# Performance work log

Measured on AMD Instinct MI355X. Metric: run time of the kernel, lower is better.

Reference implementation:

```python
import jax, jax.numpy as jnp
import numpy as np

N_NODES = 50000
N_EDGES = 800000
N_GRAPHS = 512
IN_DIM = 128
HID = 64
NLAYERS = 3
BN_EPS = 1e-5
NEG_SLOPE = 0.2


def setup_inputs() -> dict:
    key = jax.random.key(0)
    ks = jax.random.split(key, 16)
    s = 0.1  # weight scale
    x = jax.random.normal(ks[0], (N_NODES, IN_DIM), jnp.float32)
    ei_sc = jax.random.randint(ks[1], (2, N_EDGES), 0, N_NODES, dtype=jnp.int32)
    ei_fc = jax.random.randint(ks[2], (2, N_EDGES), 0, N_NODES, dtype=jnp.int32)
    batch_ids = jnp.sort(jax.random.randint(ks[3], (N_NODES,), 0, N_GRAPHS, dtype=jnp.int32))
    return {
        "x": x,
        "ei_sc": ei_sc,
        "ei_fc": ei_fc,
        "batch_ids": batch_ids,
        "Ws": jax.random.normal(ks[4], (NLAYERS, IN_DIM, 2 * HID), jnp.float32) * s,
        "att_src": jax.random.normal(ks[5], (NLAYERS, 2, HID), jnp.float32) * s,
        "att_dst": jax.random.normal(ks[6], (NLAYERS, 2, HID), jnp.float32) * s,
        "bgat": jnp.zeros((NLAYERS, 2 * HID), jnp.float32),
        "bn_g": jnp.ones((NLAYERS, 2 * HID), jnp.float32),
        "bn_b": jnp.zeros((NLAYERS, 2 * HID), jnp.float32),
        "Wf": jax.random.normal(ks[7], (2 * HID, HID), jnp.float32) * s,
        "af_src": jax.random.normal(ks[8], (1, HID), jnp.float32) * s,
        "af_dst": jax.random.normal(ks[9], (1, HID), jnp.float32) * s,
        "bf": jnp.zeros((HID,), jnp.float32),
        "Wo": jax.random.normal(ks[10], (HID, 1), jnp.float32) * s,
        "bo": jnp.zeros((1,), jnp.float32),
    }


def gat_conv(x, src, dst, W, a_src, a_dst, b):
    """PyG GATConv: linear -> per-head attention logits -> dst-segment softmax -> scatter-sum."""
    N = x.shape[0]
    H, C = a_src.shape
    h = (x @ W).reshape(N, H, C)                      # [N,H,C]
    loop = jnp.arange(N, dtype=src.dtype)             # add self-loops (PyG default)
    s = jnp.concatenate([src, loop])
    d = jnp.concatenate([dst, loop])
    al_s = jnp.einsum('nhc,hc->nh', h, a_src)         # [N,H]
    al_d = jnp.einsum('nhc,hc->nh', h, a_dst)
    al = jax.nn.leaky_relu(al_s[s] + al_d[d], NEG_SLOPE)  # [E,H]
    m = jax.ops.segment_max(al, d, num_segments=N)
    m = jnp.where(jnp.isfinite(m), m, 0.0)
    e = jnp.exp(al - m[d])
    denom = jax.ops.segment_sum(e, d, num_segments=N)
    coef = e / (denom[d] + 1e-16)                     # softmax over incoming edges
    out = jax.ops.segment_sum(coef[:, :, None] * h[s], d, num_segments=N)  # [N,H,C]
    return out.reshape(N, H * C) + b                  # concat heads + bias


def batch_norm(x, g, b):
    mu = x.mean(axis=0)
    var = ((x - mu) ** 2).mean(axis=0)                # biased var, as torch BN train-mode
    return (x - mu) * jax.lax.rsqrt(var + BN_EPS) * g + b


def reference(x, ei_sc, ei_fc, batch_ids, Ws, att_src, att_dst, bgat,
              bn_g, bn_b, Wf, af_src, af_dst, bf, Wo, bo):
    x0 = x
    x1 = x
    for l in range(NLAYERS):
        x0 = gat_conv(x0, ei_sc[0], ei_sc[1], Ws[l], att_src[l], att_dst[l], bgat[l])
        x1 = gat_conv(x1, ei_fc[0], ei_fc[1], Ws[l], att_src[l], att_dst[l], bgat[l])
        x0 = jax.nn.relu(batch_norm(x0, bn_g[l], bn_b[l]))
        x1 = jax.nn.relu(batch_norm(x1, bn_g[l], bn_b[l]))
        # Dropout: identity (eval mode, deterministic reference)
    x0 = gat_conv(x0, ei_sc[0], ei_sc[1], Wf, af_src, af_dst, bf)
    x1 = gat_conv(x1, ei_fc[0], ei_fc[1], Wf, af_src, af_dst, bf)
    xf = (x0 + x1) * 0.5                              # reduce_fuse_embed='mean'
    out = xf @ Wo + bo                                # [N, nclass]
    sums = jax.ops.segment_sum(out, batch_ids, num_segments=N_GRAPHS)
    cnts = jax.ops.segment_sum(jnp.ones((out.shape[0], 1), out.dtype), batch_ids, num_segments=N_GRAPHS)
    return sums / jnp.maximum(cnts, 1.0)              # scatter mean over graphs -> [G, nclass]
```

## Files before the change

kernel.cpp:

```cpp
#include <hip/hip_runtime.h>
#include <cstdint>
#include <cstddef>


#define NLAYERS 3
#define BN_BLOCKS 256

__device__ __forceinline__ float lrelu(float a){ return a > 0.f ? a : 0.2f*a; }

__device__ __forceinline__ float wsum(float v){
#pragma unroll
  for (int o = 32; o > 0; o >>= 1) v += __shfl_xor(v, o);
  return v;
}

__global__ void zero_k(int* __restrict__ p, int n){
  int i = blockIdx.x*blockDim.x + threadIdx.x;
  if (i < n) p[i] = 0;
}
__global__ void copy_k(const int* __restrict__ a, int* __restrict__ b, int n){
  int i = blockIdx.x*blockDim.x + threadIdx.x;
  if (i < n) b[i] = a[i];
}
__global__ void count_k(const int* __restrict__ dst, int E, int* __restrict__ cnt){
  int e = blockIdx.x*blockDim.x + threadIdx.x;
  if (e < E) atomicAdd(&cnt[dst[e]], 1);
}
__global__ __launch_bounds__(1024) void scanA_k(const int* __restrict__ cnt,
    int* __restrict__ excl, int* __restrict__ bsum, int N){
  __shared__ int wpart[16];
  const int tid = threadIdx.x, lane = tid & 63, w = tid >> 6;
  const int i = blockIdx.x*1024 + tid;
  const int v = (i < N) ? cnt[i] : 0;
  int s = v;
#pragma unroll
  for (int o = 1; o < 64; o <<= 1){ int t = __shfl_up(s, o); if (lane >= o) s += t; }
  if (lane == 63) wpart[w] = s;
  __syncthreads();
  if (w == 0){
    int t = (lane < 16) ? wpart[lane] : 0;
#pragma unroll
    for (int o = 1; o < 16; o <<= 1){ int u = __shfl_up(t, o); if (lane >= o) t += u; }
    if (lane < 16) wpart[lane] = t;
  }
  __syncthreads();
  const int woff = (w > 0) ? wpart[w-1] : 0;
  const int incl = s + woff;
  if (i < N) excl[i] = incl - v;
  if (tid == 1023) bsum[blockIdx.x] = incl;
}
__global__ void scanB_k(const int* __restrict__ bsum, int* __restrict__ boff, int nb){
  const int lane = threadIdx.x;
  const int v = (lane < nb) ? bsum[lane] : 0;
  int s = v;
#pragma unroll
  for (int o = 1; o < 64; o <<= 1){ int t = __shfl_up(s, o); if (lane >= o) s += t; }
  if (lane < nb) boff[lane] = s - v;
  if (lane == nb-1) boff[nb] = s;
}
__global__ __launch_bounds__(1024) void scanC_k(int* __restrict__ rp,
    const int* __restrict__ boff, int N, int nb){
  const int i = blockIdx.x*1024 + threadIdx.x;
  if (i < N) rp[i] += boff[blockIdx.x];
  if (i == 0) rp[N] = boff[nb];
}
__global__ void fill_k(const int* __restrict__ src, const int* __restrict__ dst, int E,
                       int* __restrict__ pos, int* __restrict__ col){
  int e = blockIdx.x*blockDim.x + threadIdx.x;
  if (e < E){
    int d = dst[e];
    int p = atomicAdd(&pos[d], 1);
    col[p] = src[e];
  }
}
__global__ __launch_bounds__(256) void sortrow_k(const int* __restrict__ rp,
                                                 int* __restrict__ col, int N){
  const int lane = threadIdx.x & 63;
  const int n = blockIdx.x*4 + (threadIdx.x >> 6);
  if (n >= N) return;
  const int b = rp[n], e = rp[n+1];
  const int deg = e - b;
  if (deg <= 1) return;
  if (deg <= 64){
    int v = (lane < deg) ? col[b + lane] : 0x7fffffff;
#pragma unroll
    for (int k = 2; k <= 64; k <<= 1){
#pragma unroll
      for (int j = k >> 1; j > 0; j >>= 1){
        const int other = __shfl_xor(v, j);
        const bool up = ((lane & k) == 0);
        const bool takeMin = (((lane & j) == 0) == up);
        v = takeMin ? min(v, other) : max(v, other);
      }
    }
    if (lane < deg) col[b + lane] = v;
  } else if (lane == 0){
    for (int i = b + 1; i < e; ++i){
      const int key = col[i];
      int j = i - 1;
      while (j >= b && col[j] > key){ col[j+1] = col[j]; --j; }
      col[j+1] = key;
    }
  }
}

__global__ __launch_bounds__(256) void gemm_k(const float* __restrict__ A,
    const float* __restrict__ W, float* __restrict__ O,
    const float* __restrict__ bnsc, const float* __restrict__ bnsh,
    const float* __restrict__ atts, const float* __restrict__ attd,
    float* __restrict__ als, float* __restrict__ ald, int N, int M){
  __shared__ float xs[64][64];
  __shared__ float wsh[64][64];
  const int tid = threadIdx.x;
  const int row0 = blockIdx.x*64, col0 = blockIdx.y*64;
  const int HS = gridDim.y;
  const int ty = tid >> 4, tx = tid & 15;
  float acc[4][4] = {};

  for (int kk = 0; kk < 128; kk += 64){
    {
      const int c4 = (tid & 15)*4;
#pragma unroll
      for (int p = 0; p < 4; ++p){
        const int k = p*16 + (tid >> 4);
        *reinterpret_cast<float4*>(&wsh[k][c4]) =
            *reinterpret_cast<const float4*>(&W[(size_t)(kk + k)*M + col0 + c4]);
      }
    }
    {
      const int k4 = (tid & 15)*4;
      const int rbase = tid >> 4;
#pragma unroll
      for (int p = 0; p < 4; ++p){
        const int rr = p*16 + rbase;
        int gr = row0 + rr; if (gr > N-1) gr = N-1;
        float4 xv = *reinterpret_cast<const float4*>(&A[(size_t)gr*128 + kk + k4]);
        float xq[4] = {xv.x, xv.y, xv.z, xv.w};
        if (bnsc != nullptr){
#pragma unroll
          for (int q = 0; q < 4; ++q)
            xq[q] = fmaxf(xq[q]*bnsc[kk + k4 + q] + bnsh[kk + k4 + q], 0.f);
        }
#pragma unroll
        for (int q = 0; q < 4; ++q){
          const int k = k4 + q;
          const int swz = ((k >> 2) & 15) << 2;
          xs[k][rr ^ swz] = xq[q];
        }
      }
    }
    __syncthreads();
#pragma unroll 8
    for (int k = 0; k < 64; ++k){
      const int swz = ((k >> 2) & 15) << 2;
      const int xr = (ty*4) ^ swz;
      const float4 xv = *reinterpret_cast<const float4*>(&xs[k][xr]);
      const float2 w0 = *reinterpret_cast<const float2*>(&wsh[k][2*tx]);
      const float2 w1 = *reinterpret_cast<const float2*>(&wsh[k][32 + 2*tx]);
      const float xq[4] = {xv.x, xv.y, xv.z, xv.w};
#pragma unroll
      for (int i = 0; i < 4; ++i){
        acc[i][0] += xq[i]*w0.x;
        acc[i][1] += xq[i]*w0.y;
        acc[i][2] += xq[i]*w1.x;
        acc[i][3] += xq[i]*w1.y;
      }
    }
    __syncthreads();
  }
  {
    const float* as = atts + col0;
    const float* ad = attd + col0;
    const float a_s0 = as[2*tx],      a_s1 = as[2*tx + 1];
    const float a_s2 = as[32 + 2*tx], a_s3 = as[33 + 2*tx];
    const float a_d0 = ad[2*tx],      a_d1 = ad[2*tx + 1];
    const float a_d2 = ad[32 + 2*tx], a_d3 = ad[33 + 2*tx];
#pragma unroll
    for (int i = 0; i < 4; ++i){
      float ps = acc[i][0]*a_s0 + acc[i][1]*a_s1 + acc[i][2]*a_s2 + acc[i][3]*a_s3;
      float pd = acc[i][0]*a_d0 + acc[i][1]*a_d1 + acc[i][2]*a_d2 + acc[i][3]*a_d3;
#pragma unroll
      for (int o = 1; o < 16; o <<= 1){
        ps += __shfl_xor(ps, o);
        pd += __shfl_xor(pd, o);
      }
      const int r = row0 + ty*4 + i;
      if (tx == 0 && r < N){
        als[(size_t)r*HS + blockIdx.y] = ps;
        ald[(size_t)r*HS + blockIdx.y] = pd;
      }
    }
  }
#pragma unroll
  for (int i = 0; i < 4; ++i){
    const int r = row0 + ty*4 + i;
    if (r < N){
      float2* o2 = reinterpret_cast<float2*>(&O[(size_t)r*M + col0]);
      o2[tx]      = make_float2(acc[i][0], acc[i][1]);
      o2[16 + tx] = make_float2(acc[i][2], acc[i][3]);
    }
  }
}

template<int H>
__global__ __launch_bounds__(256) void agg_k(const float* __restrict__ h,
    const float* __restrict__ als, const float* __restrict__ ald,
    const int* __restrict__ rp, const int* __restrict__ col,
    const float* __restrict__ bias, float* __restrict__ out, int N){
  const int lane = threadIdx.x & 63;
  const int n = blockIdx.x*4 + (threadIdx.x >> 6);
  if (n >= N) return;
  const int beg = rp[n], end = rp[n+1];
  float as0, as1 = 0.f, ad0, ad1 = 0.f;
  if (H == 2){
    const float2 a = ((const float2*)als)[n];
    const float2 d = ((const float2*)ald)[n];
    as0 = a.x; as1 = a.y; ad0 = d.x; ad1 = d.y;
  } else { as0 = als[n]; ad0 = ald[n]; }
  const float self0 = lrelu(as0 + ad0);
  const float self1 = (H == 2) ? lrelu(as1 + ad1) : 0.f;
  float m0 = self0, p0 = (lane == 0) ? 1.f : 0.f;
  float m1 = self1, p1 = (lane == 0) ? 1.f : 0.f;
  for (int i = beg + lane; i < end; i += 64){
    const int s = col[i];
    if (H == 2){
      const float2 a = ((const float2*)als)[s];
      const float al0 = lrelu(a.x + ad0);
      const float al1 = lrelu(a.y + ad1);
      if (al0 > m0){ p0 = p0*__expf(m0 - al0) + 1.f; m0 = al0; }
      else p0 += __expf(al0 - m0);
      if (al1 > m1){ p1 = p1*__expf(m1 - al1) + 1.f; m1 = al1; }
      else p1 += __expf(al1 - m1);
    } else {
      const float al0 = lrelu(als[s] + ad0);
      if (al0 > m0){ p0 = p0*__expf(m0 - al0) + 1.f; m0 = al0; }
      else p0 += __expf(al0 - m0);
    }
  }
#pragma unroll
  for (int o = 1; o < 64; o <<= 1){
    const float om0 = __shfl_xor(m0, o), op0 = __shfl_xor(p0, o);
    const float nm0 = fmaxf(m0, om0);
    p0 = p0*__expf(m0 - nm0) + op0*__expf(om0 - nm0); m0 = nm0;
    if (H == 2){
      const float om1 = __shfl_xor(m1, o), op1 = __shfl_xor(p1, o);
      const float nm1 = fmaxf(m1, om1);
      p1 = p1*__expf(m1 - nm1) + op1*__expf(om1 - nm1); m1 = nm1;
    }
  }
  const float inv0 = 1.f/(p0 + 1e-16f);
  const float inv1 = (H == 2) ? 1.f/(p1 + 1e-16f) : 0.f;

  const float4* h4 = (const float4*)h;
  if (H == 2){
    const int sub = lane & 31;
    const int half = lane >> 5;
    const float csel = (sub < 16) ? __expf(self0 - m0)*inv0 : __expf(self1 - m1)*inv1;
    const float cs = (half == 0) ? csel : 0.f;
    const float4 hv = h4[(size_t)n*32 + sub];
    float ax = cs*hv.x, ay = cs*hv.y, az = cs*hv.z, aw = cs*hv.w;
    for (int base = beg; base < end; base += 64){
      const int idx = base + lane;
      int sv = n; float c0v = 0.f, c1v = 0.f;
      if (idx < end){
        sv = col[idx];
        const float2 a = ((const float2*)als)[sv];
        c0v = __expf(lrelu(a.x + ad0) - m0)*inv0;
        c1v = __expf(lrelu(a.y + ad1) - m1)*inv1;
      }
      const int cnt = min(64, end - base);
      const int iters = (cnt + 1) >> 1;
      for (int j = 0; j < iters; ++j){
        const int e = 2*j + half;
        const int   src = __shfl(sv, e);
        const float cc0 = __shfl(c0v, e);
        const float cc1 = __shfl(c1v, e);
        const float c = (sub < 16) ? cc0 : cc1;
        const float4 hvv = h4[(size_t)src*32 + sub];
        ax += c*hvv.x; ay += c*hvv.y; az += c*hvv.z; aw += c*hvv.w;
      }
    }
    ax += __shfl_xor(ax, 32); ay += __shfl_xor(ay, 32);
    az += __shfl_xor(az, 32); aw += __shfl_xor(aw, 32);
    if (lane < 32){
      const float4 bv = ((const float4*)bias)[sub];
      float4 o4 = make_float4(ax + bv.x, ay + bv.y, az + bv.z, aw + bv.w);
      ((float4*)out)[(size_t)n*32 + sub] = o4;
    }
  } else {
    const int sub = lane & 15;
    const int quad = lane >> 4;
    const float cs = (quad == 0) ? __expf(self0 - m0)*inv0 : 0.f;
    const float4 hv = h4[(size_t)n*16 + sub];
    float ax = cs*hv.x, ay = cs*hv.y, az = cs*hv.z, aw = cs*hv.w;
    for (int base = beg; base < end; base += 64){
      const int idx = base + lane;
      int sv = n; float c0v = 0.f;
      if (idx < end){
        sv = col[idx];
        c0v = __expf(lrelu(als[sv] + ad0) - m0)*inv0;
      }
      const int cnt = min(64, end - base);
      const int iters = (cnt + 3) >> 2;
      for (int j = 0; j < iters; ++j){
        const int e = 4*j + quad;
        const int   src = __shfl(sv, e);
        const float cc  = __shfl(c0v, e);
        const float4 hvv = h4[(size_t)src*16 + sub];
        ax += cc*hvv.x; ay += cc*hvv.y; az += cc*hvv.z; aw += cc*hvv.w;
      }
    }
    ax += __shfl_xor(ax, 16); ay += __shfl_xor(ay, 16);
    az += __shfl_xor(az, 16); aw += __shfl_xor(aw, 16);
    ax += __shfl_xor(ax, 32); ay += __shfl_xor(ay, 32);
    az += __shfl_xor(az, 32); aw += __shfl_xor(aw, 32);
    if (lane < 16){
      const float4 bv = ((const float4*)bias)[sub];
      float4 o4 = make_float4(ax + bv.x, ay + bv.y, az + bv.z, aw + bv.w);
      ((float4*)out)[(size_t)n*16 + sub] = o4;
    }
  }
}

__global__ __launch_bounds__(128) void bn_stats_k(const float* __restrict__ x, int N,
                                                  double* __restrict__ part){
  const int c = threadIdx.x;
  double s = 0.0, s2 = 0.0;
  for (int r = blockIdx.x; r < N; r += gridDim.x){
    const float v = x[(size_t)r*128 + c];
    s += v; s2 += (double)v*(double)v;
  }
  part[(size_t)blockIdx.x*256 + c]       = s;
  part[(size_t)blockIdx.x*256 + 128 + c] = s2;
}
__global__ __launch_bounds__(64) void bnfin_k(const double* __restrict__ part,
    const float* __restrict__ g, const float* __restrict__ b,
    float* __restrict__ sc, float* __restrict__ sh, int N){
  const int c = blockIdx.x;
  const int l = threadIdx.x;
  double s = 0.0, s2 = 0.0;
  for (int i = l; i < BN_BLOCKS; i += 64){
    s  += part[(size_t)i*256 + c];
    s2 += part[(size_t)i*256 + 128 + c];
  }
#pragma unroll
  for (int o = 32; o > 0; o >>= 1){
    s  += __shfl_xor(s, o);
    s2 += __shfl_xor(s2, o);
  }
  if (l == 0){
    const double mu  = s/(double)N;
    const double var = s2/(double)N - mu*mu;
    const float scale = rsqrtf((float)var + 1e-5f)*g[c];
    sc[c] = scale;
    sh[c] = b[c] - (float)mu*scale;
  }
}

__global__ __launch_bounds__(256) void pred_k(const float* __restrict__ f0,
    const float* __restrict__ f1, const float* __restrict__ Wo,
    float* __restrict__ pred, int N){
  const int lane = threadIdx.x & 63;
  const int n = blockIdx.x*4 + (threadIdx.x >> 6);
  if (n >= N) return;
  const float xf = (f0[(size_t)n*64 + lane] + f1[(size_t)n*64 + lane])*0.5f;
  const float p = wsum(xf*Wo[lane]);
  if (lane == 0) pred[n] = p;
}
__global__ __launch_bounds__(64) void segred_k(const float* __restrict__ pred,
    const int* __restrict__ bid, const float* __restrict__ bo,
    float* __restrict__ out, int N){
  const int g = blockIdx.x;
  int lo = 0, hi = N;
  while (lo < hi){ const int mid = (lo + hi) >> 1; if (bid[mid] < g) lo = mid + 1; else hi = mid; }
  const int s0 = lo;
  hi = N;
  while (lo < hi){ const int mid = (lo + hi) >> 1; if (bid[mid] < g + 1) lo = mid + 1; else hi = mid; }
  const int s1 = lo;
  float s = 0.f;
  for (int i = s0 + threadIdx.x; i < s1; i += 64) s += pred[i];
  s = wsum(s);
  if (threadIdx.x == 0)
    out[g] = (s1 > s0) ? s/(float)(s1 - s0) + bo[0] : 0.f;
}

extern "C" void kernel_launch(void* const* d_in, const int* in_sizes, int n_in,
                              void* d_out, int out_size, void* d_ws, size_t ws_size,
                              hipStream_t stream) {
  const int N = in_sizes[0]/128;
  const int E = in_sizes[1]/2;
  const int G = out_size;

  const float* x    = (const float*)d_in[0];
  const int*   eisc = (const int*)d_in[1];
  const int*   eifc = (const int*)d_in[2];
  const int*   bid  = (const int*)d_in[3];
  const float* Ws   = (const float*)d_in[4];
  const float* atts = (const float*)d_in[5];
  const float* attd = (const float*)d_in[6];
  const float* bgat = (const float*)d_in[7];
  const float* bng  = (const float*)d_in[8];
  const float* bnb  = (const float*)d_in[9];
  const float* Wf   = (const float*)d_in[10];
  const float* afs  = (const float*)d_in[11];
  const float* afd  = (const float*)d_in[12];
  const float* bf   = (const float*)d_in[13];
  const float* Wo   = (const float*)d_in[14];
  const float* bo   = (const float*)d_in[15];
  float* out = (float*)d_out;

  char* wp = (char*)d_ws;
  auto grab = [&](size_t bytes)->char* {
    uintptr_t p = ((uintptr_t)wp + 255) & ~(uintptr_t)255;
    wp = (char*)(p + bytes);
    return (char*)p;
  };
  char* zbase = (char*)(((uintptr_t)d_ws + 255) & ~(uintptr_t)255);
  int*    cntA  = (int*)grab((size_t)N*4);
  int*    cntB  = (int*)grab((size_t)N*4);
  const int zwords = (int)(((size_t)(wp - zbase)) / 4);
  double* part  = (double*)grab((size_t)BN_BLOCKS*256*8);
  int*   rp_sc  = (int*)grab((size_t)(N+1)*4);
  int*   rp_fc  = (int*)grab((size_t)(N+1)*4);
  int*   col_sc = (int*)grab((size_t)E*4);
  int*   col_fc = (int*)grab((size_t)E*4);
  int*   bsum   = (int*)grab(64*4);
  int*   boff   = (int*)grab(65*4);
  float* hb     = (float*)grab((size_t)N*128*4);
  float* x0b    = (float*)grab((size_t)N*128*4);
  float* x1b    = (float*)grab((size_t)N*128*4);
  float* alsb   = (float*)grab((size_t)N*2*4);
  float* aldb   = (float*)grab((size_t)N*2*4);
  float* bnsc   = (float*)grab((size_t)6*128*4);
  float* bnsh   = (float*)grab((size_t)6*128*4);
  float* pred   = alsb;
  (void)ws_size; (void)n_in;

  zero_k<<<(zwords + 255)/256, 256, 0, stream>>>((int*)zbase, zwords);

  const int EB = (E + 255)/256;
  const int NB = (N + 255)/256;
  const int SB = (N + 1023)/1024;
  const int NB4 = (N + 3)/4;
  count_k<<<EB, 256, 0, stream>>>(eisc + E, E, cntA);
  count_k<<<EB, 256, 0, stream>>>(eifc + E, E, cntB);
  scanA_k<<<SB, 1024, 0, stream>>>(cntA, rp_sc, bsum, N);
  scanB_k<<<1, 64, 0, stream>>>(bsum, boff, SB);
  scanC_k<<<SB, 1024, 0, stream>>>(rp_sc, boff, N, SB);
  copy_k<<<NB, 256, 0, stream>>>(rp_sc, cntA, N);
  fill_k<<<EB, 256, 0, stream>>>(eisc, eisc + E, E, cntA, col_sc);
  sortrow_k<<<NB4, 256, 0, stream>>>(rp_sc, col_sc, N);
  scanA_k<<<SB, 1024, 0, stream>>>(cntB, rp_fc, bsum, N);
  scanB_k<<<1, 64, 0, stream>>>(bsum, boff, SB);
  scanC_k<<<SB, 1024, 0, stream>>>(rp_fc, boff, N, SB);
  copy_k<<<NB, 256, 0, stream>>>(rp_fc, cntB, N);
  fill_k<<<EB, 256, 0, stream>>>(eifc, eifc + E, E, cntB, col_fc);
  sortrow_k<<<NB4, 256, 0, stream>>>(rp_fc, col_fc, N);

  const dim3 gg2((N + 63)/64, 2), gg1((N + 63)/64, 1);
  const float* cur0 = x;
  const float* cur1 = x;
  for (int l = 0; l < NLAYERS; ++l){
    const float* Wl = Ws + (size_t)l*128*128;
    const float* as = atts + l*128;
    const float* ad = attd + l*128;
    const float* bg = bgat + l*128;
    const float* sc0 = (l == 0) ? nullptr : bnsc + ((l-1)*2 + 0)*128;
    const float* sh0 = (l == 0) ? nullptr : bnsh + ((l-1)*2 + 0)*128;
    const float* sc1 = (l == 0) ? nullptr : bnsc + ((l-1)*2 + 1)*128;
    const float* sh1 = (l == 0) ? nullptr : bnsh + ((l-1)*2 + 1)*128;

    gemm_k<<<gg2, 256, 0, stream>>>(cur0, Wl, hb, sc0, sh0, as, ad, alsb, aldb, N, 128);
    agg_k<2><<<NB4, 256, 0, stream>>>(hb, alsb, aldb, rp_sc, col_sc, bg, x0b, N);
    bn_stats_k<<<BN_BLOCKS, 128, 0, stream>>>(x0b, N, part);
    bnfin_k<<<128, 64, 0, stream>>>(part, bng + l*128, bnb + l*128,
                                    bnsc + (l*2 + 0)*128, bnsh + (l*2 + 0)*128, N);
    if (l != 0)
      gemm_k<<<gg2, 256, 0, stream>>>(cur1, Wl, hb, sc1, sh1, as, ad, alsb, aldb, N, 128);
    agg_k<2><<<NB4, 256, 0, stream>>>(hb, alsb, aldb, rp_fc, col_fc, bg, x1b, N);
    bn_stats_k<<<BN_BLOCKS, 128, 0, stream>>>(x1b, N, part);
    bnfin_k<<<128, 64, 0, stream>>>(part, bng + l*128, bnb + l*128,
                                    bnsc + (l*2 + 1)*128, bnsh + (l*2 + 1)*128, N);
    cur0 = x0b;
    cur1 = x1b;
  }
  gemm_k<<<gg1, 256, 0, stream>>>(cur0, Wf, hb, bnsc + 4*128, bnsh + 4*128,
                                  afs, afd, alsb, aldb, N, 64);
  agg_k<1><<<NB4, 256, 0, stream>>>(hb, alsb, aldb, rp_sc, col_sc, bf, x0b, N);

  gemm_k<<<gg1, 256, 0, stream>>>(cur1, Wf, hb, bnsc + 5*128, bnsh + 5*128,
                                  afs, afd, alsb, aldb, N, 64);
  agg_k<1><<<NB4, 256, 0, stream>>>(hb, alsb, aldb, rp_fc, col_fc, bf, x1b, N);

  pred_k<<<NB4, 256, 0, stream>>>(x0b, x1b, Wo, pred, N);
  segred_k<<<G, 64, 0, stream>>>(pred, bid, bo, out, N);
}
```

Measured before the change: 1.361 ms.

## Batch the two edge-set branches into single launches and fuse pred into segred

The two independent GAT branches (sc and fc edge sets) now run in shared launches, with a grid dimension selecting the branch. This covers CSR build, GEMM, aggregation, BN stats and BN finalize. A second h buffer and separate attention-logit buffers are allocated when the workspace is large enough; otherwise the code falls back to sequential per-branch launches. The per-node prediction kernel is removed, and segred now averages the features of both branches and takes the dot product with Wo directly. The aim is to halve the number of launches and give the GPU wider grids. The cost is extra workspace and a serial per-graph node loop in segred.

```diff
diff --git a/kernel.cpp b/kernel.cpp
--- a/kernel.cpp
+++ b/kernel.cpp
@@ -18,16 +18,19 @@
   int i = blockIdx.x*blockDim.x + threadIdx.x;
   if (i < n) p[i] = 0;
 }
-__global__ void copy_k(const int* __restrict__ a, int* __restrict__ b, int n){
-  int i = blockIdx.x*blockDim.x + threadIdx.x;
-  if (i < n) b[i] = a[i];
-}
-__global__ void count_k(const int* __restrict__ dst, int E, int* __restrict__ cnt){
-  int e = blockIdx.x*blockDim.x + threadIdx.x;
-  if (e < E) atomicAdd(&cnt[dst[e]], 1);
-}
-__global__ __launch_bounds__(1024) void scanA_k(const int* __restrict__ cnt,
-    int* __restrict__ excl, int* __restrict__ bsum, int N){
+__global__ void count2_k(const int* __restrict__ d0, const int* __restrict__ d1,
+                         int E, int* __restrict__ c0, int* __restrict__ c1){
+  const int e = blockIdx.x*blockDim.x + threadIdx.x;
+  const int* d = blockIdx.y ? d1 : d0;
+  int* c = blockIdx.y ? c1 : c0;
+  if (e < E) atomicAdd(&c[d[e]], 1);
+}
+__global__ __launch_bounds__(1024) void scanA2_k(const int* __restrict__ c0,
+    const int* __restrict__ c1, int* __restrict__ r0, int* __restrict__ r1,
+    int* __restrict__ bsum, int N){
+  const int z = blockIdx.y;
+  const int* cnt = z ? c1 : c0;
+  int* excl = z ? r1 : r0;
   __shared__ int wpart[16];
   const int tid = threadIdx.x, lane = tid & 63, w = tid >> 6;
   const int i = blockIdx.x*1024 + tid;
@@ -47,34 +50,50 @@
   const int woff = (w > 0) ? wpart[w-1] : 0;
   const int incl = s + woff;
   if (i < N) excl[i] = incl - v;
-  if (tid == 1023) bsum[blockIdx.x] = incl;
-}
-__global__ void scanB_k(const int* __restrict__ bsum, int* __restrict__ boff, int nb){
+  if (tid == 1023) bsum[z*64 + blockIdx.x] = incl;
+}
+__global__ void scanB2_k(const int* __restrict__ bsum, int* __restrict__ boff, int nb){
+  const int z = blockIdx.y;
   const int lane = threadIdx.x;
-  const int v = (lane < nb) ? bsum[lane] : 0;
+  const int v = (lane < nb) ? bsum[z*64 + lane] : 0;
   int s = v;
 #pragma unroll
   for (int o = 1; o < 64; o <<= 1){ int t = __shfl_up(s, o); if (lane >= o) s += t; }
-  if (lane < nb) boff[lane] = s - v;
-  if (lane == nb-1) boff[nb] = s;
-}
-__global__ __launch_bounds__(1024) void scanC_k(int* __restrict__ rp,
+  if (lane < nb) boff[z*65 + lane] = s - v;
+  if (lane == nb-1) boff[z*65 + nb] = s;
+}
+__global__ __launch_bounds__(1024) void scanC2_k(int* __restrict__ r0,
+    int* __restrict__ r1, int* __restrict__ p0, int* __restrict__ p1,
     const int* __restrict__ boff, int N, int nb){
+  const int z = blockIdx.y;
+  int* rp  = z ? r1 : r0;
+  int* pos = z ? p1 : p0;
   const int i = blockIdx.x*1024 + threadIdx.x;
-  if (i < N) rp[i] += boff[blockIdx.x];
-  if (i == 0) rp[N] = boff[nb];
-}
-__global__ void fill_k(const int* __restrict__ src, const int* __restrict__ dst, int E,
-                       int* __restrict__ pos, int* __restrict__ col){
-  int e = blockIdx.x*blockDim.x + threadIdx.x;
+  if (i < N){
+    const int v = rp[i] + boff[z*65 + blockIdx.x];
+    rp[i] = v;
+    pos[i] = v;
+  }
+  if (i == 0) rp[N] = boff[z*65 + nb];
+}
+__global__ void fill2_k(const int* __restrict__ e0, const int* __restrict__ e1,
+    int E, int* __restrict__ p0, int* __restrict__ p1,
+    int* __restrict__ col0, int* __restrict__ col1){
+  const int e = blockIdx.x*blockDim.x + threadIdx.x;
+  const int* ei = blockIdx.y ? e1 : e0;
+  int* pos = blockIdx.y ? p1 : p0;
+  int* col = blockIdx.y ? col1 : col0;
   if (e < E){
-    int d = dst[e];
-    int p = atomicAdd(&pos[d], 1);
-    col[p] = src[e];
-  }
-}
-__global__ __launch_bounds__(256) void sortrow_k(const int* __restrict__ rp,
-                                                 int* __restrict__ col, int N){
+    const int d = ei[E + e];
+    const int p = atomicAdd(&pos[d], 1);
+    col[p] = ei[e];
+  }
+}
+__global__ __launch_bounds__(256) void sortrow2_k(const int* __restrict__ r0,
+    const int* __restrict__ r1, int* __restrict__ c0, int* __restrict__ c1, int N){
+  const int z = blockIdx.y;
+  const int* rp = z ? r1 : r0;
+  int* col = z ? c1 : c0;
   const int lane = threadIdx.x & 63;
   const int n = blockIdx.x*4 + (threadIdx.x >> 6);
   if (n >= N) return;
@@ -104,11 +123,23 @@
   }
 }
 
-__global__ __launch_bounds__(256) void gemm_k(const float* __restrict__ A,
-    const float* __restrict__ W, float* __restrict__ O,
-    const float* __restrict__ bnsc, const float* __restrict__ bnsh,
+__global__ __launch_bounds__(256) void gemm_k(
+    const float* __restrict__ A0, const float* __restrict__ A1,
+    const float* __restrict__ W, float* __restrict__ O0, float* __restrict__ O1,
+    const float* __restrict__ scA, const float* __restrict__ shA,
+    const float* __restrict__ scB, const float* __restrict__ shB,
     const float* __restrict__ atts, const float* __restrict__ attd,
-    float* __restrict__ als, float* __restrict__ ald, int N, int M){
+    float* __restrict__ als0, float* __restrict__ ald0,
+    float* __restrict__ als1, float* __restrict__ ald1,
+    int N, int M, int zbase){
+  const int br = blockIdx.z + zbase;
+  const float* A = br ? A1 : A0;
+  float* O = br ? O1 : O0;
+  const float* bnsc = br ? scB : scA;
+  const float* bnsh = br ? shB : shA;
+  float* als = br ? als1 : als0;
+  float* ald = br ? ald1 : ald0;
+
   __shared__ float xs[64][64];
   __shared__ float wsh[64][64];
   const int tid = threadIdx.x;
@@ -203,10 +234,22 @@
 }
 
 template<int H>
-__global__ __launch_bounds__(256) void agg_k(const float* __restrict__ h,
-    const float* __restrict__ als, const float* __restrict__ ald,
-    const int* __restrict__ rp, const int* __restrict__ col,
-    const float* __restrict__ bias, float* __restrict__ out, int N){
+__global__ __launch_bounds__(256) void agg_k(
+    const float* __restrict__ h0, const float* __restrict__ h1,
+    const float* __restrict__ als0A, const float* __restrict__ ald0A,
+    const float* __restrict__ als1A, const float* __restrict__ ald1A,
+    const int* __restrict__ rp0, const int* __restrict__ col0A,
+    const int* __restrict__ rp1, const int* __restrict__ col1A,
+    const float* __restrict__ bias, float* __restrict__ out0,
+    float* __restrict__ out1, int N, int zbase){
+  const int br = blockIdx.y + zbase;
+  const float* h   = br ? h1 : h0;
+  const float* als = br ? als1A : als0A;
+  const float* ald = br ? ald1A : ald0A;
+  const int* rp  = br ? rp1 : rp0;
+  const int* col = br ? col1A : col0A;
+  float* out = br ? out1 : out0;
+
   const int lane = threadIdx.x & 63;
   const int n = blockIdx.x*4 + (threadIdx.x >> 6);
   if (n >= N) return;
@@ -284,8 +327,8 @@
     az += __shfl_xor(az, 32); aw += __shfl_xor(aw, 32);
     if (lane < 32){
       const float4 bv = ((const float4*)bias)[sub];
-      float4 o4 = make_float4(ax + bv.x, ay + bv.y, az + bv.z, aw + bv.w);
-      ((float4*)out)[(size_t)n*32 + sub] = o4;
+      ((float4*)out)[(size_t)n*32 + sub] =
+          make_float4(ax + bv.x, ay + bv.y, az + bv.z, aw + bv.w);
     }
   } else {
     const int sub = lane & 15;
@@ -316,32 +359,36 @@
     az += __shfl_xor(az, 32); aw += __shfl_xor(aw, 32);
     if (lane < 16){
       const float4 bv = ((const float4*)bias)[sub];
-      float4 o4 = make_float4(ax + bv.x, ay + bv.y, az + bv.z, aw + bv.w);
-      ((float4*)out)[(size_t)n*16 + sub] = o4;
-    }
-  }
-}
-
-__global__ __launch_bounds__(128) void bn_stats_k(const float* __restrict__ x, int N,
-                                                  double* __restrict__ part){
+      ((float4*)out)[(size_t)n*16 + sub] =
+          make_float4(ax + bv.x, ay + bv.y, az + bv.z, aw + bv.w);
+    }
+  }
+}
+
+__global__ __launch_bounds__(128) void bn_stats2_k(const float* __restrict__ x0,
+    const float* __restrict__ x1, int N, double* __restrict__ part){
+  const int z = blockIdx.y;
+  const float* x = z ? x1 : x0;
+  double* p = part + (size_t)z*BN_BLOCKS*256;
   const int c = threadIdx.x;
   double s = 0.0, s2 = 0.0;
   for (int r = blockIdx.x; r < N; r += gridDim.x){
     const float v = x[(size_t)r*128 + c];
     s += v; s2 += (double)v*(double)v;
   }
-  part[(size_t)blockIdx.x*256 + c]       = s;
-  part[(size_t)blockIdx.x*256 + 128 + c] = s2;
-}
-__global__ __launch_bounds__(64) void bnfin_k(const double* __restrict__ part,
+  p[(size_t)blockIdx.x*256 + c]       = s;
+  p[(size_t)blockIdx.x*256 + 128 + c] = s2;
+}
+__global__ __launch_bounds__(64) void bnfin2_k(const double* __restrict__ part,
     const float* __restrict__ g, const float* __restrict__ b,
     float* __restrict__ sc, float* __restrict__ sh, int N){
-  const int c = blockIdx.x;
+  const int c = blockIdx.x, z = blockIdx.y;
   const int l = threadIdx.x;
+  const double* p = part + (size_t)z*BN_BLOCKS*256;
   double s = 0.0, s2 = 0.0;
   for (int i = l; i < BN_BLOCKS; i += 64){
-    s  += part[(size_t)i*256 + c];
-    s2 += part[(size_t)i*256 + 128 + c];
+    s  += p[(size_t)i*256 + c];
+    s2 += p[(size_t)i*256 + 128 + c];
   }
 #pragma unroll
   for (int o = 32; o > 0; o >>= 1){
@@ -352,36 +399,29 @@
     const double mu  = s/(double)N;
     const double var = s2/(double)N - mu*mu;
     const float scale = rsqrtf((float)var + 1e-5f)*g[c];
-    sc[c] = scale;
-    sh[c] = b[c] - (float)mu*scale;
-  }
-}
-
-__global__ __launch_bounds__(256) void pred_k(const float* __restrict__ f0,
+    sc[z*128 + c] = scale;
+    sh[z*128 + c] = b[c] - (float)mu*scale;
+  }
+}
+
+__global__ __launch_bounds__(64) void segred_k(const float* __restrict__ f0,
     const float* __restrict__ f1, const float* __restrict__ Wo,
-    float* __restrict__ pred, int N){
-  const int lane = threadIdx.x & 63;
-  const int n = blockIdx.x*4 + (threadIdx.x >> 6);
-  if (n >= N) return;
-  const float xf = (f0[(size_t)n*64 + lane] + f1[(size_t)n*64 + lane])*0.5f;
-  const float p = wsum(xf*Wo[lane]);
-  if (lane == 0) pred[n] = p;
-}
-__global__ __launch_bounds__(64) void segred_k(const float* __restrict__ pred,
-    const int* __restrict__ bid, const float* __restrict__ bo,
+    const float* __restrict__ bo, const int* __restrict__ bid,
     float* __restrict__ out, int N){
   const int g = blockIdx.x;
+  const int lane = threadIdx.x;
   int lo = 0, hi = N;
   while (lo < hi){ const int mid = (lo + hi) >> 1; if (bid[mid] < g) lo = mid + 1; else hi = mid; }
   const int s0 = lo;
   hi = N;
   while (lo < hi){ const int mid = (lo + hi) >> 1; if (bid[mid] < g + 1) lo = mid + 1; else hi = mid; }
   const int s1 = lo;
-  float s = 0.f;
-  for (int i = s0 + threadIdx.x; i < s1; i += 64) s += pred[i];
-  s = wsum(s);
-  if (threadIdx.x == 0)
-    out[g] = (s1 > s0) ? s/(float)(s1 - s0) + bo[0] : 0.f;
+  float acc = 0.f;
+  for (int i = s0; i < s1; ++i)
+    acc += f0[(size_t)i*64 + lane] + f1[(size_t)i*64 + lane];
+  const float p = wsum(acc*0.5f*Wo[lane]);
+  if (lane == 0)
+    out[g] = (s1 > s0) ? p/(float)(s1 - s0) + bo[0] : 0.f;
 }
 
 extern "C" void kernel_launch(void* const* d_in, const int* in_sizes, int n_in,
@@ -419,45 +459,40 @@
   int*    cntA  = (int*)grab((size_t)N*4);
   int*    cntB  = (int*)grab((size_t)N*4);
   const int zwords = (int)(((size_t)(wp - zbase)) / 4);
-  double* part  = (double*)grab((size_t)BN_BLOCKS*256*8);
+  double* part  = (double*)grab((size_t)2*BN_BLOCKS*256*8);
   int*   rp_sc  = (int*)grab((size_t)(N+1)*4);
   int*   rp_fc  = (int*)grab((size_t)(N+1)*4);
   int*   col_sc = (int*)grab((size_t)E*4);
   int*   col_fc = (int*)grab((size_t)E*4);
-  int*   bsum   = (int*)grab(64*4);
-  int*   boff   = (int*)grab(65*4);
-  float* hb     = (float*)grab((size_t)N*128*4);
+  int*   bsum   = (int*)grab(128*4);
+  int*   boff   = (int*)grab(130*4);
+  float* hb0    = (float*)grab((size_t)N*128*4);
   float* x0b    = (float*)grab((size_t)N*128*4);
   float* x1b    = (float*)grab((size_t)N*128*4);
-  float* alsb   = (float*)grab((size_t)N*2*4);
-  float* aldb   = (float*)grab((size_t)N*2*4);
+  float* als0   = (float*)grab((size_t)N*2*4);
+  float* ald0   = (float*)grab((size_t)N*2*4);
+  float* als1   = (float*)grab((size_t)N*2*4);
+  float* ald1   = (float*)grab((size_t)N*2*4);
   float* bnsc   = (float*)grab((size_t)6*128*4);
   float* bnsh   = (float*)grab((size_t)6*128*4);
-  float* pred   = alsb;
-  (void)ws_size; (void)n_in;
+  char*  hb1_p  = grab((size_t)N*128*4);
+  const size_t needed = (size_t)(wp - (char*)d_ws);
+  const bool big = (ws_size >= needed);
+  float* hb1 = big ? (float*)hb1_p : hb0;
+  (void)n_in;
 
   zero_k<<<(zwords + 255)/256, 256, 0, stream>>>((int*)zbase, zwords);
 
   const int EB = (E + 255)/256;
-  const int NB = (N + 255)/256;
   const int SB = (N + 1023)/1024;
   const int NB4 = (N + 3)/4;
-  count_k<<<EB, 256, 0, stream>>>(eisc + E, E, cntA);
-  count_k<<<EB, 256, 0, stream>>>(eifc + E, E, cntB);
-  scanA_k<<<SB, 1024, 0, stream>>>(cntA, rp_sc, bsum, N);
-  scanB_k<<<1, 64, 0, stream>>>(bsum, boff, SB);
-  scanC_k<<<SB, 1024, 0, stream>>>(rp_sc, boff, N, SB);
-  copy_k<<<NB, 256, 0, stream>>>(rp_sc, cntA, N);
-  fill_k<<<EB, 256, 0, stream>>>(eisc, eisc + E, E, cntA, col_sc);
-  sortrow_k<<<NB4, 256, 0, stream>>>(rp_sc, col_sc, N);
-  scanA_k<<<SB, 1024, 0, stream>>>(cntB, rp_fc, bsum, N);
-  scanB_k<<<1, 64, 0, stream>>>(bsum, boff, SB);
-  scanC_k<<<SB, 1024, 0, stream>>>(rp_fc, boff, N, SB);
-  copy_k<<<NB, 256, 0, stream>>>(rp_fc, cntB, N);
-  fill_k<<<EB, 256, 0, stream>>>(eifc, eifc + E, E, cntB, col_fc);
-  sortrow_k<<<NB4, 256, 0, stream>>>(rp_fc, col_fc, N);
-
-  const dim3 gg2((N + 63)/64, 2), gg1((N + 63)/64, 1);
+  count2_k<<<dim3(EB,2), 256, 0, stream>>>(eisc + E, eifc + E, E, cntA, cntB);
+  scanA2_k<<<dim3(SB,2), 1024, 0, stream>>>(cntA, cntB, rp_sc, rp_fc, bsum, N);
+  scanB2_k<<<dim3(1,2), 64, 0, stream>>>(bsum, boff, SB);
+  scanC2_k<<<dim3(SB,2), 1024, 0, stream>>>(rp_sc, rp_fc, cntA, cntB, boff, N, SB);
+  fill2_k<<<dim3(EB,2), 256, 0, stream>>>(eisc, eifc, E, cntA, cntB, col_sc, col_fc);
+  sortrow2_k<<<dim3(NB4,2), 256, 0, stream>>>(rp_sc, rp_fc, col_sc, col_fc, N);
+
   const float* cur0 = x;
   const float* cur1 = x;
   for (int l = 0; l < NLAYERS; ++l){
@@ -465,33 +500,67 @@
     const float* as = atts + l*128;
     const float* ad = attd + l*128;
     const float* bg = bgat + l*128;
-    const float* sc0 = (l == 0) ? nullptr : bnsc + ((l-1)*2 + 0)*128;
-    const float* sh0 = (l == 0) ? nullptr : bnsh + ((l-1)*2 + 0)*128;
-    const float* sc1 = (l == 0) ? nullptr : bnsc + ((l-1)*2 + 1)*128;
-    const float* sh1 = (l == 0) ? nullptr : bnsh + ((l-1)*2 + 1)*128;
-
-    gemm_k<<<gg2, 256, 0, stream>>>(cur0, Wl, hb, sc0, sh0, as, ad, alsb, aldb, N, 128);
-    agg_k<2><<<NB4, 256, 0, stream>>>(hb, alsb, aldb, rp_sc, col_sc, bg, x0b, N);
-    bn_stats_k<<<BN_BLOCKS, 128, 0, stream>>>(x0b, N, part);
-    bnfin_k<<<128, 64, 0, stream>>>(part, bng + l*128, bnb + l*128,
-                                    bnsc + (l*2 + 0)*128, bnsh + (l*2 + 0)*128, N);
-    if (l != 0)
-      gemm_k<<<gg2, 256, 0, stream>>>(cur1, Wl, hb, sc1, sh1, as, ad, alsb, aldb, N, 128);
-    agg_k<2><<<NB4, 256, 0, stream>>>(hb, alsb, aldb, rp_fc, col_fc, bg, x1b, N);
-    bn_stats_k<<<BN_BLOCKS, 128, 0, stream>>>(x1b, N, part);
-    bnfin_k<<<128, 64, 0, stream>>>(part, bng + l*128, bnb + l*128,
-                                    bnsc + (l*2 + 1)*128, bnsh + (l*2 + 1)*128, N);
+    const float* scA = (l == 0) ? nullptr : bnsc + ((l-1)*2 + 0)*128;
+    const float* shA = (l == 0) ? nullptr : bnsh + ((l-1)*2 + 0)*128;
+    const float* scB = (l == 0) ? nullptr : bnsc + ((l-1)*2 + 1)*128;
+    const float* shB = (l == 0) ? nullptr : bnsh + ((l-1)*2 + 1)*128;
+
+    if (l == 0){
+      gemm_k<<<dim3((N+63)/64, 2, 1), 256, 0, stream>>>(
+          x, x, Wl, hb0, hb0, nullptr, nullptr, nullptr, nullptr,
+          as, ad, als0, ald0, als0, ald0, N, 128, 0);
+      if (big){
+        agg_k<2><<<dim3(NB4, 2), 256, 0, stream>>>(hb0, hb0, als0, ald0, als0, ald0,
+            rp_sc, col_sc, rp_fc, col_fc, bg, x0b, x1b, N, 0);
+      } else {
+        agg_k<2><<<dim3(NB4, 1), 256, 0, stream>>>(hb0, hb0, als0, ald0, als0, ald0,
+            rp_sc, col_sc, rp_fc, col_fc, bg, x0b, x1b, N, 0);
+        agg_k<2><<<dim3(NB4, 1), 256, 0, stream>>>(hb0, hb0, als0, ald0, als0, ald0,
+            rp_sc, col_sc, rp_fc, col_fc, bg, x0b, x1b, N, 1);
+      }
+    } else if (big){
+      gemm_k<<<dim3((N+63)/64, 2, 2), 256, 0, stream>>>(
+          cur0, cur1, Wl, hb0, hb1, scA, shA, scB, shB,
+          as, ad, als0, ald0, als1, ald1, N, 128, 0);
+      agg_k<2><<<dim3(NB4, 2), 256, 0, stream>>>(hb0, hb1, als0, ald0, als1, ald1,
+          rp_sc, col_sc, rp_fc, col_fc, bg, x0b, x1b, N, 0);
+    } else {
+      gemm_k<<<dim3((N+63)/64, 2, 1), 256, 0, stream>>>(
+          cur0, cur1, Wl, hb0, hb1, scA, shA, scB, shB,
+          as, ad, als0, ald0, als1, ald1, N, 128, 0);
+      agg_k<2><<<dim3(NB4, 1), 256, 0, stream>>>(hb0, hb1, als0, ald0, als1, ald1,
+          rp_sc, col_sc, rp_fc, col_fc, bg, x0b, x1b, N, 0);
+      gemm_k<<<dim3((N+63)/64, 2, 1), 256, 0, stream>>>(
+          cur0, cur1, Wl, hb0, hb1, scA, shA, scB, shB,
+          as, ad, als0, ald0, als1, ald1, N, 128, 1);
+      agg_k<2><<<dim3(NB4, 1), 256, 0, stream>>>(hb0, hb1, als0, ald0, als1, ald1,
+          rp_sc, col_sc, rp_fc, col_fc, bg, x0b, x1b, N, 1);
+    }
+    bn_stats2_k<<<dim3(BN_BLOCKS, 2), 128, 0, stream>>>(x0b, x1b, N, part);
+    bnfin2_k<<<dim3(128, 2), 64, 0, stream>>>(part, bng + l*128, bnb + l*128,
+                                              bnsc + l*2*128, bnsh + l*2*128, N);
     cur0 = x0b;
     cur1 = x1b;
   }
-  gemm_k<<<gg1, 256, 0, stream>>>(cur0, Wf, hb, bnsc + 4*128, bnsh + 4*128,
-                                  afs, afd, alsb, aldb, N, 64);
-  agg_k<1><<<NB4, 256, 0, stream>>>(hb, alsb, aldb, rp_sc, col_sc, bf, x0b, N);
-
-  gemm_k<<<gg1, 256, 0, stream>>>(cur1, Wf, hb, bnsc + 5*128, bnsh + 5*128,
-                                  afs, afd, alsb, aldb, N, 64);
-  agg_k<1><<<NB4, 256, 0, stream>>>(hb, alsb, aldb, rp_fc, col_fc, bf, x1b, N);
-
-  pred_k<<<NB4, 256, 0, stream>>>(x0b, x1b, Wo, pred, N);
-  segred_k<<<G, 64, 0, stream>>>(pred, bid, bo, out, N);
-}
+  const float* scA = bnsc + 4*128, *shA = bnsh + 4*128;
+  const float* scB = bnsc + 5*128, *shB = bnsh + 5*128;
+  if (big){
+    gemm_k<<<dim3((N+63)/64, 1, 2), 256, 0, stream>>>(
+        cur0, cur1, Wf, hb0, hb1, scA, shA, scB, shB,
+        afs, afd, als0, ald0, als1, ald1, N, 64, 0);
+    agg_k<1><<<dim3(NB4, 2), 256, 0, stream>>>(hb0, hb1, als0, ald0, als1, ald1,
+        rp_sc, col_sc, rp_fc, col_fc, bf, x0b, x1b, N, 0);
+  } else {
+    gemm_k<<<dim3((N+63)/64, 1, 1), 256, 0, stream>>>(
+        cur0, cur1, Wf, hb0, hb1, scA, shA, scB, shB,
+        afs, afd, als0, ald0, als1, ald1, N, 64, 0);
+    agg_k<1><<<dim3(NB4, 1), 256, 0, stream>>>(hb0, hb1, als0, ald0, als1, ald1,
+        rp_sc, col_sc, rp_fc, col_fc, bf, x0b, x1b, N, 0);
+    gemm_k<<<dim3((N+63)/64, 1, 1), 256, 0, stream>>>(
+        cur0, cur1, Wf, hb0, hb1, scA, shA, scB, shB,
+        afs, afd, als0, ald0, als1, ald1, N, 64, 1);
+    agg_k<1><<<dim3(NB4, 1), 256, 0, stream>>>(hb0, hb1, als0, ald0, als1, ald1,
+        rp_sc, col_sc, rp_fc, col_fc, bf, x0b, x1b, N, 1);
+  }
+  segred_k<<<G, 64, 0, stream>>>(x0b, x1b, Wo, bo, bid, out, N);
+}
```

New measurement: 1.168 ms. 1.17x faster.
